# Kernel tuning notes

Measured on AMD Instinct MI355X. Metric: run time of the kernel, lower is better.

The kernel has to match this reference:

```python
import math
import jax, jax.numpy as jnp
import numpy as np

HEADS = 16


def setup_inputs() -> dict:
    key = jax.random.key(0)
    k1, k2, k3, k4, k5 = jax.random.split(key, 5)
    B, S, D = 2, 2048, 1024
    return {
        "x": jax.random.normal(k1, (B, S, D), dtype=jnp.float32),
        "Wqkv": jax.random.normal(k2, (3 * D, D), dtype=jnp.float32) * (1.0 / math.sqrt(D)),
        "bqkv": jax.random.normal(k3, (3 * D,), dtype=jnp.float32) * 0.02,
        "Wo": jax.random.normal(k4, (D, D), dtype=jnp.float32) * (1.0 / math.sqrt(D)),
        "bo": jax.random.normal(k5, (D,), dtype=jnp.float32) * 0.02,
    }


def reference(x, Wqkv, bqkv, Wo, bo):
    B, S, D = x.shape
    H = HEADS
    hd = D // H  # head dim
    qkv = x @ Wqkv.T + bqkv                      # (B, S, 3D)
    # Faithful to torch: direct contiguous reshape (NOT a transpose-based head split)
    qkv = qkv.reshape(B, H, S, 3 * hd)           # (B, H, S, 3*hd)
    q, k, v = jnp.split(qkv, 3, axis=-1)         # each (B, H, S, hd)
    scores = jnp.einsum("bhsd,bhtd->bhst", q, k) * (1.0 / math.sqrt(hd))
    attn = jax.nn.softmax(scores, axis=-1)       # (B, H, S, S)
    vals = jnp.einsum("bhst,bhtd->bhsd", attn, v)
    vals = vals.reshape(B, S, D)                 # faithful direct reshape back
    return vals @ Wo.T + bo
```

## Files before the change

kernel.cpp:

```cpp
#include <hip/hip_runtime.h>
#include <stdint.h>

typedef unsigned short u16;
typedef __attribute__((ext_vector_type(8))) short short8;
typedef __attribute__((ext_vector_type(4))) float f32x4;
typedef __attribute__((ext_vector_type(16))) float f32x16;
typedef __attribute__((ext_vector_type(8))) __bf16 bf16x8;
typedef __attribute__((ext_vector_type(4))) unsigned u32x4;

#define DEV static __device__ __forceinline__

template <typename T>
DEV auto mfma_try(T a, T b, f32x4 c, int)
    -> decltype(__builtin_amdgcn_mfma_f32_16x16x32_bf16(a, b, c, 0, 0, 0)) {
  return __builtin_amdgcn_mfma_f32_16x16x32_bf16(a, b, c, 0, 0, 0);
}
template <typename T>
DEV f32x4 mfma_try(T a, T b, f32x4 c, long) {
  return __builtin_amdgcn_mfma_f32_16x16x32_bf16(
      __builtin_bit_cast(bf16x8, a), __builtin_bit_cast(bf16x8, b), c, 0, 0, 0);
}
DEV f32x4 MFMA(short8 a, short8 b, f32x4 c) { return mfma_try(a, b, c, 0); }

template <typename T>
DEV auto mfma32_try(T a, T b, f32x16 c, int)
    -> decltype(__builtin_amdgcn_mfma_f32_32x32x16_bf16(a, b, c, 0, 0, 0)) {
  return __builtin_amdgcn_mfma_f32_32x32x16_bf16(a, b, c, 0, 0, 0);
}
template <typename T>
DEV f32x16 mfma32_try(T a, T b, f32x16 c, long) {
  return __builtin_amdgcn_mfma_f32_32x32x16_bf16(
      __builtin_bit_cast(bf16x8, a), __builtin_bit_cast(bf16x8, b), c, 0, 0, 0);
}
DEV f32x16 MFMA32(short8 a, short8 b, f32x16 c) { return mfma32_try(a, b, c, 0); }

DEV void gload16(const u16* g, u16* lds) {
  __builtin_amdgcn_global_load_lds((unsigned int*)g, (unsigned int*)lds, 16, 0, 0);
}

DEV u16 f2bf(float f) {
  unsigned u = __float_as_uint(f);
  u = (u + 0x7FFFu + ((u >> 16) & 1u)) >> 16;
  return (u16)u;
}

DEV float exp2fast(float x) {
  float r;
  asm("v_exp_f32 %0, %1" : "=v"(r) : "v"(x));
  return r;
}

DEV unsigned cvtpk_bf16(float lo, float hi_) {
  unsigned r;
  asm("v_cvt_pk_bf16_f32 %0, %1, %2" : "=v"(r) : "v"(lo), "v"(hi_));
  return r;
}

DEV void permswap(unsigned& a, unsigned& b) {
  asm volatile("v_permlane32_swap_b32 %0, %1" : "+v"(a), "+v"(b));
}

__global__ void cvt_kernel(const float* __restrict__ x, const float* __restrict__ wq,
                           const float* __restrict__ wo, u16* __restrict__ xb,
                           u16* __restrict__ wqb, u16* __restrict__ wob) {
  const int N1 = 4194304 / 4, N2 = 3145728 / 4, N3 = 1048576 / 4;
  const int total = N1 + N2 + N3;
  for (int i = blockIdx.x * blockDim.x + threadIdx.x; i < total;
       i += gridDim.x * blockDim.x) {
    const float4* s;
    u16* d;
    int off;
    if (i < N1) { s = (const float4*)x; d = xb; off = i; }
    else if (i < N1 + N2) { s = (const float4*)wq; d = wqb; off = i - N1; }
    else { s = (const float4*)wo; d = wob; off = i - N1 - N2; }
    float4 v = s[off];
    ushort4 o;
    o.x = f2bf(v.x); o.y = f2bf(v.y); o.z = f2bf(v.z); o.w = f2bf(v.w);
    ((ushort4*)d)[off] = o;
  }
}

__global__ __launch_bounds__(512, 2) void gemm1_256(
    const u16* __restrict__ A, const u16* __restrict__ Bm,
    const float* __restrict__ bias,
    u16* __restrict__ Qb, u16* __restrict__ Kb, u16* __restrict__ Vb) {
  extern __shared__ __align__(16) u16 sm[];
  const int tid = threadIdx.x;
  const int lane = tid & 63;
  const int wave = tid >> 6;
  const int wr = wave >> 2, wc = wave & 3;
  const int l15 = lane & 15, l4 = lane >> 4;

  const int bid = blockIdx.x;
  const int wg = (bid & 7) * 24 + (bid >> 3);
  const int by = wg / 12, bx = wg - (wg / 12) * 12;
  const int m0 = by * 256, n0 = bx * 256;

  f32x4 acc[8][4] = {};

  auto stage = [&](int dbuf, int t) {
#pragma unroll
    for (int i = 0; i < 4; ++i) {
      const int Il = i * 512 + tid;
      const int r = Il >> 3, bb = Il & 7;
      gload16(A + ((size_t)(m0 + r) << 10) + t * 64 + ((bb ^ (r & 7)) << 3),
              sm + (dbuf * 4096 + Il) * 8);
    }
#pragma unroll
    for (int i = 0; i < 4; ++i) {
      const int Il = i * 512 + tid;
      const int r = Il >> 3, bb = Il & 7;
      gload16(Bm + ((size_t)(n0 + r) << 10) + t * 64 + ((bb ^ (r & 7)) << 3),
              sm + (dbuf * 4096 + 2048 + Il) * 8);
    }
  };

  stage(0, 0);
  for (int t = 0; t < 16; ++t) {
    const int cur = t & 1;
    if (t + 1 < 16) {
      stage(cur ^ 1, t + 1);
      asm volatile("s_waitcnt vmcnt(8)" ::: "memory");
    } else {
      asm volatile("s_waitcnt vmcnt(0)" ::: "memory");
    }
    __builtin_amdgcn_s_barrier();

    const u16* base = sm + cur * 32768;
#pragma unroll
    for (int kk = 0; kk < 2; ++kk) {
      short8 af[8], bf[4];
#pragma unroll
      for (int mi = 0; mi < 8; ++mi) {
        const int r = wr * 128 + mi * 16 + l15;
        af[mi] =
            *(const short8*)(base + ((r << 3) + ((kk * 4 + l4) ^ (r & 7))) * 8);
      }
#pragma unroll
      for (int nj = 0; nj < 4; ++nj) {
        const int r = wc * 64 + nj * 16 + l15;
        bf[nj] = *(const short8*)(base +
                                  (2048 + (r << 3) + ((kk * 4 + l4) ^ (r & 7))) * 8);
      }
      __builtin_amdgcn_s_setprio(1);
#pragma unroll
      for (int mi = 0; mi < 8; ++mi)
#pragma unroll
        for (int nj = 0; nj < 4; ++nj)
          acc[mi][nj] = MFMA(af[mi], bf[nj], acc[mi][nj]);
      __builtin_amdgcn_s_setprio(0);
    }
    __builtin_amdgcn_s_barrier();
  }

#pragma unroll
  for (int nj = 0; nj < 4; ++nj) {
    const int c = n0 + wc * 64 + nj * 16 + l15;
    const float bv = bias[c];
    const int chunk = c / 192;
    const int tt = c - chunk * 192;
    const int sel = tt >> 6;
    const int dd = tt & 63;
    u16* dst = (sel == 0) ? Qb : ((sel == 1) ? Kb : Vb);
#pragma unroll
    for (int mi = 0; mi < 8; ++mi)
#pragma unroll
      for (int r = 0; r < 4; ++r) {
        const int mm = m0 + wr * 128 + mi * 16 + l4 * 4 + r;
        const u16 bfv = f2bf(acc[mi][nj][r] + bv);
        const int bb2 = mm >> 11;
        const int s = mm & 2047;
        const int s2 = (s & 127) * 16 + chunk;
        const int bh = bb2 * 16 + (s >> 7);
        dst[((size_t)bh * 2048 + s2) * 64 + dd] = bfv;
      }
  }
}

__global__ __launch_bounds__(256, 2) void gemm_bt(
    const u16* __restrict__ A, const u16* __restrict__ Bm,
    const float* __restrict__ bias, float* __restrict__ Cf, int M, int N, int K) {
  __shared__ u16 As[128 * 32];
  __shared__ u16 Bs[128 * 32];
  const int tid = threadIdx.x;
  const int lane = tid & 63;
  const int wave = tid >> 6;
  const int wr = wave >> 1, wc = wave & 1;
  const int l15 = lane & 15, l4 = lane >> 4;
  const int m0 = blockIdx.y * 128, n0 = blockIdx.x * 128;

  f32x4 acc[4][4] = {};

  const u16* ga = A + (size_t)(m0 + (tid >> 2)) * K + (tid & 3) * 8;
  const u16* gb = Bm + (size_t)(n0 + (tid >> 2)) * K + (tid & 3) * 8;
  u16* la = As + tid * 8;
  u16* lb = Bs + tid * 8;
  const size_t rstep = (size_t)64 * K;

  for (int kt = 0; kt < K; kt += 32) {
    gload16(ga + kt, la);
    gload16(ga + kt + rstep, la + 2048);
    gload16(gb + kt, lb);
    gload16(gb + kt + rstep, lb + 2048);
    __syncthreads();
    short8 af[4], bfr[4];
#pragma unroll
    for (int i = 0; i < 4; ++i)
      af[i] = *(const short8*)(As + (wr * 64 + i * 16 + l15) * 32 + l4 * 8);
#pragma unroll
    for (int i = 0; i < 4; ++i)
      bfr[i] = *(const short8*)(Bs + (wc * 64 + i * 16 + l15) * 32 + l4 * 8);
#pragma unroll
    for (int i = 0; i < 4; ++i)
#pragma unroll
      for (int j = 0; j < 4; ++j) acc[i][j] = MFMA(af[i], bfr[j], acc[i][j]);
    __syncthreads();
  }

#pragma unroll
  for (int nj = 0; nj < 4; ++nj) {
    const int c = n0 + wc * 64 + nj * 16 + l15;
    const float bv = bias[c];
#pragma unroll
    for (int mi = 0; mi < 4; ++mi)
#pragma unroll
      for (int r = 0; r < 4; ++r) {
        const int m = m0 + wr * 64 + mi * 16 + l4 * 4 + r;
        Cf[(size_t)m * N + c] = acc[mi][nj][r] + bv;
      }
  }
}

__global__ __launch_bounds__(256) void vtrans_kernel(const u16* __restrict__ Vn,
                                                     u16* __restrict__ VT) {
  __shared__ u16 T[64 * 72];
  const int tid = threadIdx.x;
  const int bh = blockIdx.x >> 5;
  const int s0 = (blockIdx.x & 31) * 64;
  const int r = tid >> 3, c8 = tid & 7;
#pragma unroll
  for (int i = 0; i < 2; ++i) {
    const int s = r + i * 32;
    short8 v = *(const short8*)(Vn + ((size_t)bh * 2048 + s0 + s) * 64 + c8 * 8);
#pragma unroll
    for (int j = 0; j < 8; ++j) T[(c8 * 8 + j) * 72 + s] = (u16)v[j];
  }
  __syncthreads();
#pragma unroll
  for (int i = 0; i < 2; ++i) {
    const int d = (tid >> 3) + i * 32;
    short8 v = *(const short8*)(&T[d * 72 + (tid & 7) * 8]);
    *(short8*)(VT + ((size_t)bh * 64 + d) * 2048 + s0 + (tid & 7) * 8) = v;
  }
}

__global__ __launch_bounds__(512) void attn_kernel(
    const u16* __restrict__ Qg, const u16* __restrict__ Kg,
    const u16* __restrict__ VTg, u16* __restrict__ v2) {
  __shared__ __align__(16) char smem[65536];
  u16* const KS = (u16*)smem;
  u16* const VS = (u16*)smem + 16384;
  float* const FM = (float*)smem;

  const int tid = threadIdx.x;
  const int lane = tid & 63;
  const int half = tid >> 8;
  const int tid256 = tid & 255;
  const int w4 = (tid >> 6) & 3;
  const int l31 = lane & 31;
  const int hi = lane >> 5;

  const int bid = blockIdx.x;
  const int logical = (bid & 7) * 64 + (bid >> 3);
  const int bh = logical >> 4;
  const int qt = logical & 15;

  const u16* Qh = Qg + (size_t)bh * 2048 * 64;
  const u16* Kh = Kg + (size_t)bh * 2048 * 64;
  const u16* VTh = VTg + (size_t)bh * 64 * 2048;

  const int q0 = qt * 128 + w4 * 32;
  const float C1 = 0.18033688f;

  short8 qf[4];
#pragma unroll
  for (int d_ = 0; d_ < 4; ++d_)
    qf[d_] = *(const short8*)(Qh + (size_t)(q0 + l31) * 64 + d_ * 16 + hi * 8);

  f32x16 ot[2] = {};
  float ls4[4] = {0.f, 0.f, 0.f, 0.f};

  const int r8 = tid256 >> 3;
  const int c16 = tid256 & 7;
  const int xr = l31 & 7;
  const int Tbase = half * 16;

  auto stage = [&](int buf, int T) {
    u16* kd = KS + (half * 2 + buf) * 4096 + tid256 * 8;
    u16* vd = VS + (half * 2 + buf) * 4096 + tid256 * 8;
#pragma unroll
    for (int i = 0; i < 2; ++i) {
      const int row = i * 32 + r8;
      gload16(Kh + (size_t)(T * 64 + row) * 64 + ((c16 ^ (row & 7)) * 8),
              kd + i * 2048);
    }
#pragma unroll
    for (int i = 0; i < 2; ++i) {
      const int d = i * 32 + r8;
      gload16(VTh + (size_t)d * 2048 + T * 64 + ((c16 ^ (d & 7)) * 8),
              vd + i * 2048);
    }
  };

  stage(0, Tbase);
  __syncthreads();

  for (int t = 0; t < 16; ++t) {
    const int cur = t & 1;
    if (t + 1 < 16) stage(cur ^ 1, Tbase + t + 1);

    const u16* Kb = KS + (half * 2 + cur) * 4096;
    const u16* Vb = VS + (half * 2 + cur) * 4096;

    f32x16 st[2] = {};
    __builtin_amdgcn_s_setprio(1);
#pragma unroll
    for (int n = 0; n < 2; ++n)
#pragma unroll
      for (int d_ = 0; d_ < 4; ++d_) {
        short8 kf = *(const short8*)(Kb + (n * 32 + l31) * 64 +
                                     (((d_ * 2 + hi) ^ xr) * 8));
        st[n] = MFMA32(kf, qf[d_], st[n]);
      }
    __builtin_amdgcn_s_setprio(0);

    float p0[16], p1[16];
#pragma unroll
    for (int r = 0; r < 16; ++r) {
      p0[r] = exp2fast(st[0][r] * C1);
      p1[r] = exp2fast(st[1][r] * C1);
    }
#pragma unroll
    for (int i = 0; i < 4; ++i)
      ls4[i] += ((p0[i] + p0[i + 4]) + (p0[i + 8] + p0[i + 12])) +
                ((p1[i] + p1[i + 4]) + (p1[i + 8] + p1[i + 12]));

    short8 pf[2][2];
#pragma unroll
    for (int n = 0; n < 2; ++n) {
      const float* p = n ? p1 : p0;
      unsigned W[4][2];
#pragma unroll
      for (int j = 0; j < 4; ++j)
#pragma unroll
        for (int pp = 0; pp < 2; ++pp)
          W[j][pp] = cvtpk_bf16(p[4 * j + 2 * pp], p[4 * j + 2 * pp + 1]);
#pragma unroll
      for (int ks = 0; ks < 2; ++ks) {
        unsigned x0 = W[2 * ks][0], y0 = W[2 * ks + 1][0];
        unsigned x1 = W[2 * ks][1], y1 = W[2 * ks + 1][1];
        permswap(x0, y0);
        permswap(x1, y1);
        u32x4 pw = {x0, x1, y0, y1};
        pf[n][ks] = __builtin_bit_cast(short8, pw);
      }
    }

    __builtin_amdgcn_s_setprio(1);
#pragma unroll
    for (int db = 0; db < 2; ++db)
#pragma unroll
      for (int ksg = 0; ksg < 4; ++ksg) {
        short8 vf = *(const short8*)(Vb + (db * 32 + l31) * 64 +
                                     (((ksg * 2 + hi) ^ xr) * 8));
        ot[db] = MFMA32(vf, pf[ksg >> 1][ksg & 1], ot[db]);
      }
    __builtin_amdgcn_s_setprio(0);

    __syncthreads();
  }

  float l = (ls4[0] + ls4[1]) + (ls4[2] + ls4[3]);
  l += __shfl_xor(l, 32);

  if (half == 1) {
    float* F = FM + (size_t)(w4 * 64 + lane) * 33;
#pragma unroll
    for (int r = 0; r < 16; ++r) {
      F[r] = ot[0][r];
      F[16 + r] = ot[1][r];
    }
    F[32] = l;
  }
  __syncthreads();
  if (half == 0) {
    const float* F = FM + (size_t)(w4 * 64 + lane) * 33;
    const float inv = 1.0f / (l + F[32]);

    const int s2v = q0 + l31;
    const int rowO = (bh >> 4) * 2048 + (bh & 15) * 128 + (s2v >> 4);
    const int colb = (s2v & 15) * 64;
#pragma unroll
    for (int db = 0; db < 2; ++db)
#pragma unroll
      for (int g = 0; g < 4; ++g) {
        ushort4 w;
        w.x = f2bf((ot[db][4 * g + 0] + F[db * 16 + 4 * g + 0]) * inv);
        w.y = f2bf((ot[db][4 * g + 1] + F[db * 16 + 4 * g + 1]) * inv);
        w.z = f2bf((ot[db][4 * g + 2] + F[db * 16 + 4 * g + 2]) * inv);
        w.w = f2bf((ot[db][4 * g + 3] + F[db * 16 + 4 * g + 3]) * inv);
        const int d = db * 32 + 8 * g + 4 * hi;
        *(ushort4*)(v2 + (size_t)rowO * 1024 + colb + d) = w;
      }
  }
}

extern "C" void kernel_launch(void* const* d_in, const int* in_sizes, int n_in,
                              void* d_out, int out_size, void* d_ws, size_t ws_size,
                              hipStream_t stream) {
  const float* x = (const float*)d_in[0];
  const float* Wqkv = (const float*)d_in[1];
  const float* bqkv = (const float*)d_in[2];
  const float* Wo = (const float*)d_in[3];
  const float* bo = (const float*)d_in[4];
  float* out = (float*)d_out;

  char* ws = (char*)d_ws;
  u16* xb   = (u16*)(ws);
  u16* wqb  = (u16*)(ws + 8388608);
  u16* wob  = (u16*)(ws + 14680064);
  u16* Qb   = (u16*)(ws + 16777216);
  u16* Kb   = (u16*)(ws + 25165824);
  u16* VTb  = (u16*)(ws + 33554432);
  u16* v2   = (u16*)(ws + 41943040);
  u16* Vnat = v2;

  cvt_kernel<<<2048, 256, 0, stream>>>(x, Wqkv, Wo, xb, wqb, wob);

  hipFuncSetAttribute((const void*)gemm1_256,
                      hipFuncAttributeMaxDynamicSharedMemorySize, 131072);
  gemm1_256<<<192, 512, 131072, stream>>>(xb, wqb, bqkv, Qb, Kb, Vnat);

  vtrans_kernel<<<1024, 256, 0, stream>>>(Vnat, VTb);

  attn_kernel<<<512, 512, 0, stream>>>(Qb, Kb, VTb, v2);

  dim3 g2(8, 32);
  gemm_bt<<<g2, 256, 0, stream>>>(v2, wob, bo, out, 4096, 1024, 1024);
}
```

Baseline: 121.5 us.

## Replace 256x256 QKV GEMM with 128x128 tiles and LDS-staged coalesced epilogue

The QKV projection GEMM moves from a 256x256 tile with 512 threads, double-buffered XOR-swizzled LDS and 128KB dynamic shared memory to a simpler 128x128 tile with 256 threads and single-buffered static LDS. This gives 768 blocks instead of 192 and higher occupancy. The epilogue now stages bf16 results in padded shared memory and writes contiguous 64-element rows with 16-byte stores, replacing the old scattered 2-byte stores. In exchange it loses load/compute overlap, shared-memory swizzling (risking bank conflicts) and per-block data reuse.

```diff
diff --git a/kernel.cpp b/kernel.cpp
--- a/kernel.cpp
+++ b/kernel.cpp
@@ -80,101 +80,78 @@
   }
 }
 
-__global__ __launch_bounds__(512, 2) void gemm1_256(
+__global__ __launch_bounds__(256, 4) void gemm1_128(
     const u16* __restrict__ A, const u16* __restrict__ Bm,
     const float* __restrict__ bias,
     u16* __restrict__ Qb, u16* __restrict__ Kb, u16* __restrict__ Vb) {
-  extern __shared__ __align__(16) u16 sm[];
+  __shared__ u16 SM[128 * 136];
+  u16* const As = SM;
+  u16* const Bs = SM + 4096;
+  const int K = 1024;
   const int tid = threadIdx.x;
   const int lane = tid & 63;
   const int wave = tid >> 6;
-  const int wr = wave >> 2, wc = wave & 3;
+  const int wr = wave >> 1, wc = wave & 1;
   const int l15 = lane & 15, l4 = lane >> 4;
-
-  const int bid = blockIdx.x;
-  const int wg = (bid & 7) * 24 + (bid >> 3);
-  const int by = wg / 12, bx = wg - (wg / 12) * 12;
-  const int m0 = by * 256, n0 = bx * 256;
-
-  f32x4 acc[8][4] = {};
-
-  auto stage = [&](int dbuf, int t) {
-#pragma unroll
-    for (int i = 0; i < 4; ++i) {
-      const int Il = i * 512 + tid;
-      const int r = Il >> 3, bb = Il & 7;
-      gload16(A + ((size_t)(m0 + r) << 10) + t * 64 + ((bb ^ (r & 7)) << 3),
-              sm + (dbuf * 4096 + Il) * 8);
-    }
-#pragma unroll
-    for (int i = 0; i < 4; ++i) {
-      const int Il = i * 512 + tid;
-      const int r = Il >> 3, bb = Il & 7;
-      gload16(Bm + ((size_t)(n0 + r) << 10) + t * 64 + ((bb ^ (r & 7)) << 3),
-              sm + (dbuf * 4096 + 2048 + Il) * 8);
-    }
-  };
-
-  stage(0, 0);
-  for (int t = 0; t < 16; ++t) {
-    const int cur = t & 1;
-    if (t + 1 < 16) {
-      stage(cur ^ 1, t + 1);
-      asm volatile("s_waitcnt vmcnt(8)" ::: "memory");
-    } else {
-      asm volatile("s_waitcnt vmcnt(0)" ::: "memory");
-    }
-    __builtin_amdgcn_s_barrier();
-
-    const u16* base = sm + cur * 32768;
-#pragma unroll
-    for (int kk = 0; kk < 2; ++kk) {
-      short8 af[8], bf[4];
-#pragma unroll
-      for (int mi = 0; mi < 8; ++mi) {
-        const int r = wr * 128 + mi * 16 + l15;
-        af[mi] =
-            *(const short8*)(base + ((r << 3) + ((kk * 4 + l4) ^ (r & 7))) * 8);
-      }
-#pragma unroll
-      for (int nj = 0; nj < 4; ++nj) {
-        const int r = wc * 64 + nj * 16 + l15;
-        bf[nj] = *(const short8*)(base +
-                                  (2048 + (r << 3) + ((kk * 4 + l4) ^ (r & 7))) * 8);
-      }
-      __builtin_amdgcn_s_setprio(1);
-#pragma unroll
-      for (int mi = 0; mi < 8; ++mi)
-#pragma unroll
-        for (int nj = 0; nj < 4; ++nj)
-          acc[mi][nj] = MFMA(af[mi], bf[nj], acc[mi][nj]);
-      __builtin_amdgcn_s_setprio(0);
-    }
-    __builtin_amdgcn_s_barrier();
+  const int m0 = blockIdx.y * 128, n0 = blockIdx.x * 128;
+
+  f32x4 acc[4][4] = {};
+
+  const u16* ga = A + (size_t)(m0 + (tid >> 2)) * K + (tid & 3) * 8;
+  const u16* gb = Bm + (size_t)(n0 + (tid >> 2)) * K + (tid & 3) * 8;
+  u16* la = As + tid * 8;
+  u16* lb = Bs + tid * 8;
+  const size_t rstep = (size_t)64 * K;
+
+  for (int kt = 0; kt < K; kt += 32) {
+    gload16(ga + kt, la);
+    gload16(ga + kt + rstep, la + 2048);
+    gload16(gb + kt, lb);
+    gload16(gb + kt + rstep, lb + 2048);
+    __syncthreads();
+    short8 af[4], bfr[4];
+#pragma unroll
+    for (int i = 0; i < 4; ++i)
+      af[i] = *(const short8*)(As + (wr * 64 + i * 16 + l15) * 32 + l4 * 8);
+#pragma unroll
+    for (int i = 0; i < 4; ++i)
+      bfr[i] = *(const short8*)(Bs + (wc * 64 + i * 16 + l15) * 32 + l4 * 8);
+#pragma unroll
+    for (int i = 0; i < 4; ++i)
+#pragma unroll
+      for (int j = 0; j < 4; ++j) acc[i][j] = MFMA(af[i], bfr[j], acc[i][j]);
+    __syncthreads();
   }
 
 #pragma unroll
   for (int nj = 0; nj < 4; ++nj) {
-    const int c = n0 + wc * 64 + nj * 16 + l15;
-    const float bv = bias[c];
-    const int chunk = c / 192;
-    const int tt = c - chunk * 192;
-    const int sel = tt >> 6;
-    const int dd = tt & 63;
-    u16* dst = (sel == 0) ? Qb : ((sel == 1) ? Kb : Vb);
-#pragma unroll
-    for (int mi = 0; mi < 8; ++mi)
+    const int cl = wc * 64 + nj * 16 + l15;
+    const float bv = bias[n0 + cl];
+#pragma unroll
+    for (int mi = 0; mi < 4; ++mi)
 #pragma unroll
       for (int r = 0; r < 4; ++r) {
-        const int mm = m0 + wr * 128 + mi * 16 + l4 * 4 + r;
-        const u16 bfv = f2bf(acc[mi][nj][r] + bv);
-        const int bb2 = mm >> 11;
-        const int s = mm & 2047;
-        const int s2 = (s & 127) * 16 + chunk;
-        const int bh = bb2 * 16 + (s >> 7);
-        dst[((size_t)bh * 2048 + s2) * 64 + dd] = bfv;
-      }
-  }
+        const int ml = wr * 64 + mi * 16 + l4 * 4 + r;
+        SM[ml * 136 + cl] = f2bf(acc[mi][nj][r] + bv);
+      }
+  }
+  __syncthreads();
+
+  const int ml = tid >> 1;
+  const int h = tid & 1;
+  const int m = m0 + ml;
+  const int c0 = n0 + h * 64;
+  const int chunk = c0 / 192;
+  const int sel = (c0 - chunk * 192) >> 6;
+  u16* const dst = (sel == 0) ? Qb : ((sel == 1) ? Kb : Vb);
+  const int s = m & 2047;
+  const int bh = (m >> 11) * 16 + (s >> 7);
+  const int s2 = (s & 127) * 16 + chunk;
+  u16* const drow = dst + ((size_t)bh * 2048 + s2) * 64;
+  const u16* const srow = SM + ml * 136 + h * 64;
+#pragma unroll
+  for (int g = 0; g < 8; ++g)
+    *(short8*)(drow + g * 8) = *(const short8*)(srow + g * 8);
 }
 
 __global__ __launch_bounds__(256, 2) void gemm_bt(
@@ -437,9 +414,8 @@
 
   cvt_kernel<<<2048, 256, 0, stream>>>(x, Wqkv, Wo, xb, wqb, wob);
 
-  hipFuncSetAttribute((const void*)gemm1_256,
-                      hipFuncAttributeMaxDynamicSharedMemorySize, 131072);
-  gemm1_256<<<192, 512, 131072, stream>>>(xb, wqb, bqkv, Qb, Kb, Vnat);
+  dim3 g1(24, 32);
+  gemm1_128<<<g1, 256, 0, stream>>>(xb, wqb, bqkv, Qb, Kb, Vnat);
 
   vtrans_kernel<<<1024, 256, 0, stream>>>(Vnat, VTb);
 
```

Result: slower. 124.4 us (+2.4%).
